# Kernel tuning notes

Hardware: AMD Instinct MI355X
Metric: run time of the kernel (lower is better)

## Reference

```python
import jax, jax.numpy as jnp
import numpy as np

NEG_SLOPE_GAT = 0.2   # GATConv internal leaky_relu slope (PyG default)
NEG_SLOPE = 0.01      # nn.LeakyReLU default slope


def _gat(h_src_in, h_dst_in, src, dst, Wsrc, Wdst, a_s, a_d, b, n_dst, self_loops):
    """Single-head PyG-style GATConv: gather -> score -> edge softmax -> scatter-sum."""
    hs = h_src_in @ Wsrc            # [N_src, C]
    hd = h_dst_in @ Wdst            # [N_dst, C]
    if self_loops:                  # static flag; same node set on both sides
        loop = jnp.arange(n_dst, dtype=src.dtype)
        src = jnp.concatenate([src, loop])
        dst = jnp.concatenate([dst, loop])
    # attention logits per edge
    e = jax.nn.leaky_relu((hs @ a_s)[src] + (hd @ a_d)[dst], NEG_SLOPE_GAT)  # [E]
    # softmax over edges sharing a destination node
    m = jax.ops.segment_max(e, dst, num_segments=n_dst)
    ex = jnp.exp(e - m[dst])
    denom = jax.ops.segment_sum(ex, dst, num_segments=n_dst)
    alpha = ex / denom[dst]
    out = jax.ops.segment_sum(hs[src] * alpha[:, None], dst, num_segments=n_dst)
    return out + b


def setup_inputs() -> dict:
    key = jax.random.key(0)
    ks = iter(jax.random.split(key, 64))
    NB, NP = 100_000, 50_000
    E_bb, E_pp, E_bp = 800_000, 400_000, 400_000
    FB, FP, H, H2 = 32, 34, 64, 32
    rn = lambda shape, s=0.05: jax.random.normal(next(ks), shape, jnp.float32) * s
    d = {}
    d['x_b'] = rn((NB, FB), 1.0)
    d['x_p'] = rn((NP, FP), 1.0)
    d['ei_bb'] = jax.random.randint(next(ks), (2, E_bb), 0, NB, jnp.int32)
    d['ei_pp'] = jax.random.randint(next(ks), (2, E_pp), 0, NP, jnp.int32)
    d['ei_bp_src'] = jax.random.randint(next(ks), (E_bp,), 0, NB, jnp.int32)
    d['ei_bp_dst'] = jax.random.randint(next(ks), (E_bp,), 0, NP, jnp.int32)
    d['W_in_b'] = rn((FB, H)); d['b_in_b'] = jnp.zeros((H,), jnp.float32)
    d['W_in_p'] = rn((FP, H)); d['b_in_p'] = jnp.zeros((H,), jnp.float32)
    for tag, cin, cout in (('1', H, H), ('2', H, H2)):
        d['W_bb' + tag] = rn((cin, cout)); d['as_bb' + tag] = rn((cout,)); d['ad_bb' + tag] = rn((cout,)); d['b_bb' + tag] = jnp.zeros((cout,), jnp.float32)
        d['W_pp' + tag] = rn((cin, cout)); d['as_pp' + tag] = rn((cout,)); d['ad_pp' + tag] = rn((cout,)); d['b_pp' + tag] = jnp.zeros((cout,), jnp.float32)
        d['Ws_bp' + tag] = rn((cin, cout)); d['Wd_bp' + tag] = rn((cin, cout)); d['as_bp' + tag] = rn((cout,)); d['ad_bp' + tag] = rn((cout,)); d['b_bp' + tag] = jnp.zeros((cout,), jnp.float32)
    d['W_out'] = rn((H2, 1)); d['b_out'] = jnp.zeros((1,), jnp.float32)
    return d


def reference(x_b, x_p, ei_bb, ei_pp, ei_bp_src, ei_bp_dst,
              W_in_b, b_in_b, W_in_p, b_in_p,
              W_bb1, as_bb1, ad_bb1, b_bb1, W_pp1, as_pp1, ad_pp1, b_pp1,
              Ws_bp1, Wd_bp1, as_bp1, ad_bp1, b_bp1,
              W_bb2, as_bb2, ad_bb2, b_bb2, W_pp2, as_pp2, ad_pp2, b_pp2,
              Ws_bp2, Wd_bp2, as_bp2, ad_bp2, b_bp2,
              W_out, b_out):
    NB, NP = x_b.shape[0], x_p.shape[0]
    lr = lambda v: jax.nn.leaky_relu(v, NEG_SLOPE)
    # input projections (dropout is eval-mode identity)
    hb = lr(x_b @ W_in_b + b_in_b)
    hp = lr(x_p @ W_in_p + b_in_p)
    # hetero conv 1 (sum aggregation over relations sharing a dst type)
    ob = _gat(hb, hb, ei_bb[0], ei_bb[1], W_bb1, W_bb1, as_bb1, ad_bb1, b_bb1, NB, True)
    op = (_gat(hp, hp, ei_pp[0], ei_pp[1], W_pp1, W_pp1, as_pp1, ad_pp1, b_pp1, NP, True)
          + _gat(hb, hp, ei_bp_src, ei_bp_dst, Ws_bp1, Wd_bp1, as_bp1, ad_bp1, b_bp1, NP, False))
    hb, hp = lr(ob), lr(op)
    # hetero conv 2
    ob2 = _gat(hb, hb, ei_bb[0], ei_bb[1], W_bb2, W_bb2, as_bb2, ad_bb2, b_bb2, NB, True)
    op2 = (_gat(hp, hp, ei_pp[0], ei_pp[1], W_pp2, W_pp2, as_pp2, ad_pp2, b_pp2, NP, True)
           + _gat(hb, hp, ei_bp_src, ei_bp_dst, Ws_bp2, Wd_bp2, as_bp2, ad_bp2, b_bp2, NP, False))
    hp = lr(op2)
    return hp @ W_out + b_out  # [NP, 1]
```

## Files before the change

kernel.cpp:

```cpp
#include <hip/hip_runtime.h>
#include <hip/hip_bf16.h>
#include <cstdint>
#include <cstddef>


typedef __attribute__((ext_vector_type(8))) short short8;
typedef __attribute__((ext_vector_type(4))) float f32x4;
typedef unsigned int u32;
typedef __hip_bfloat16 bf16;

#define ABITS 9
#define CHUNKE 8192

static __device__ __forceinline__ float ldf(const void* p, int i, int bf) {
    return bf ? __bfloat162float(((const bf16*)p)[i]) : ((const float*)p)[i];
}

static __device__ __forceinline__ short f2bs(float f) {
    bf16 h = __float2bfloat16(f);
    return *reinterpret_cast<short*>(&h);
}
static __device__ __forceinline__ float bs2f(short s) {
    bf16 h = *reinterpret_cast<bf16*>(&s);
    return __bfloat162float(h);
}
static __device__ __forceinline__ float lo16(u32 u) { return bs2f((short)(u & 0xffffu)); }
static __device__ __forceinline__ float hi16(u32 u) { return bs2f((short)(u >> 16)); }
static __device__ __forceinline__ u32 pack2(float x, float y) {
    return (u32)(unsigned short)f2bs(x) | ((u32)(unsigned short)f2bs(y) << 16);
}
static __device__ __forceinline__ float sel4(const float* a, int i) {
    return i == 0 ? a[0] : i == 1 ? a[1] : i == 2 ? a[2] : a[3];
}
static __device__ __forceinline__ float lrelu2(float x) { return x > 0.f ? x : 0.2f * x; }

static __device__ __forceinline__ int probe_bf(const unsigned* __restrict__ w, int* cnt) {
    if (threadIdx.x == 0) *cnt = 0;
    __syncthreads();
    int c = 0;
#pragma unroll
    for (int j = 0; j < 4; ++j) {
        unsigned u = w[threadIdx.x * 4 + j];
        unsigned e = (u >> 7) & 0xffu;
        c += (e >= 100u && e <= 145u) ? 1 : 0;
    }
    atomicAdd(cnt, c);
    __syncthreads();
    int r = (*cnt > 614) ? 1 : 0;
    __syncthreads();
    return r;
}

__global__ __launch_bounds__(256) void k_fv(
    const unsigned* __restrict__ probe_w, int* __restrict__ flag,
    const void* W_bb1, const void* as_bb1, const void* ad_bb1,
    const void* Ws_bp1, const void* as_bp1,
    const void* W_pp1, const void* as_pp1, const void* ad_pp1,
    const void* Wd_bp1, const void* ad_bp1,
    float* __restrict__ FVg)
{
    __shared__ int cnt;
    int bf = probe_bf(probe_w, &cnt);
    if (threadIdx.x == 0) *flag = bf;
    int lane = threadIdx.x & 63, wv = threadIdx.x >> 6;
    const void* Ws[6] = { W_bb1, W_bb1, Ws_bp1, W_pp1, W_pp1, Wd_bp1 };
    const void* av[6] = { as_bb1, ad_bb1, as_bp1, as_pp1, ad_pp1, ad_bp1 };
#pragma unroll
    for (int v = 0; v < 6; ++v) {
        float a = ldf(av[v], lane, bf);
        for (int k = wv; k < 64; k += 4) {
            float p = ldf(Ws[v], k * 64 + lane, bf) * a;
#pragma unroll
            for (int off = 1; off < 64; off <<= 1) p += __shfl_xor(p, off);
            if (lane == 0) FVg[v * 64 + k] = p;
        }
    }
}

template <int CIN>
static __device__ __forceinline__ void in_proj_body(
    short* WT, float* bl, float* FV, int bid,
    const void* __restrict__ X, const void* __restrict__ W, const void* __restrict__ B,
    const float* __restrict__ FVg,
    bf16* __restrict__ Y,
    float* __restrict__ S0, float* __restrict__ S1v, float* __restrict__ S2v,
    int M, int bf)
{
    constexpr int KP = 40;
    for (int i = threadIdx.x; i < 64 * CIN; i += 256) {
        int n = i / CIN, k = i - n * CIN;
        WT[n * KP + k] = f2bs(ldf(W, k * 64 + n, bf));
    }
    if (threadIdx.x < 64) bl[threadIdx.x] = ldf(B, threadIdx.x, bf);
    if (threadIdx.x < 192) FV[threadIdx.x] = FVg[threadIdx.x];
    __syncthreads();

    int lane = threadIdx.x & 63;
    int wv   = threadIdx.x >> 6;
    int m = lane & 15, quad = lane >> 4;
    int row0 = (bid * 4 + wv) * 16;
    if (row0 >= M) return;

    int arow = row0 + m; if (arow >= M) arow = M - 1;
    short8 a;
#pragma unroll
    for (int j = 0; j < 8; ++j)
        a[j] = f2bs(ldf(X, arow * CIN + quad * 8 + j, bf));

    f32x4 acc[4] = {};
#pragma unroll
    for (int tt = 0; tt < 4; ++tt) {
        short8 bfr = *(const short8*)&WT[((lane & 15) + 16 * tt) * KP + quad * 8];
        acc[tt] = __builtin_amdgcn_mfma_f32_16x16x32_bf16(a, bfr, acc[tt], 0, 0, 0);
    }

    if (CIN == 34) {
        float x32[4], x33[4];
#pragma unroll
        for (int r = 0; r < 4; ++r) {
            int row = row0 + quad * 4 + r; if (row >= M) row = M - 1;
            x32[r] = ldf(X, row * CIN + 32, bf);
            x33[r] = ldf(X, row * CIN + 33, bf);
        }
#pragma unroll
        for (int tt = 0; tt < 4; ++tt) {
            int col = (lane & 15) + 16 * tt;
            float w32 = bs2f(WT[col * KP + 32]);
            float w33 = bs2f(WT[col * KP + 33]);
#pragma unroll
            for (int r = 0; r < 4; ++r)
                acc[tt][r] += x32[r] * w32 + x33[r] * w33;
        }
    }

    float vs[4] = {}, vd[4] = {}, ve[4] = {};
#pragma unroll
    for (int tt = 0; tt < 4; ++tt) {
        int col = (lane & 15) + 16 * tt;
        float bb = bl[col];
        float w0 = FV[col], w1 = FV[64 + col], w2 = FV[128 + col];
#pragma unroll
        for (int r = 0; r < 4; ++r) {
            int row = row0 + quad * 4 + r;
            float v = acc[tt][r] + bb;
            v = v > 0.f ? v : 0.01f * v;
            if (row < M) Y[(size_t)row * 64 + col] = __float2bfloat16(v);
            vs[r] += v * w0; vd[r] += v * w1; ve[r] += v * w2;
        }
    }
#pragma unroll
    for (int off = 1; off < 16; off <<= 1)
#pragma unroll
        for (int r = 0; r < 4; ++r) {
            vs[r] += __shfl_xor(vs[r], off);
            vd[r] += __shfl_xor(vd[r], off);
            ve[r] += __shfl_xor(ve[r], off);
        }
    int c = lane & 15;
    int row = row0 + quad * 4 + (c & 3);
    if (row < M && c < 12) {
        if (c < 4)       S0[row]  = sel4(vs, c & 3);
        else if (c < 8)  S1v[row] = sel4(vd, c & 3);
        else             S2v[row] = sel4(ve, c & 3);
    }
}

__global__ __launch_bounds__(256) void k_hist_projp(
    const int* __restrict__ bb_d, const int* __restrict__ pp_d,
    const int* __restrict__ bp_d, int* __restrict__ histM,
    int E_bb, int E_pp, int E_bp, int NB, int NP, int nbkt, int nblk,
    const void* __restrict__ Xp, const void* __restrict__ Wp, const void* __restrict__ Bp,
    bf16* __restrict__ Yp, int MP,
    const float* __restrict__ FVg, const int* __restrict__ flag,
    float* __restrict__ ss_pp, float* __restrict__ sd_pp, float* __restrict__ sd_bp)
{
    __shared__ short WT[64 * 40];
    __shared__ float bl[64];
    __shared__ float FV[192];
    __shared__ int aux[1 << ABITS];
    if ((int)blockIdx.x < nblk) {
        for (int i = threadIdx.x; i < nbkt; i += 256) aux[i] = 0;
        __syncthreads();
        int E_all = E_bb + E_pp + E_bp;
        int base = blockIdx.x * CHUNKE;
        int end = base + CHUNKE < E_all ? base + CHUNKE : E_all;
        for (int i = base + threadIdx.x; i < end; i += 256) {
            int d;
            if (i < E_bb) d = bb_d[i];
            else if (i < E_bb + E_pp) d = NB + pp_d[i - E_bb];
            else d = NB + NP + bp_d[i - E_bb - E_pp];
            atomicAdd(&aux[d >> ABITS], 1);
        }
        __syncthreads();
        for (int i = threadIdx.x; i < nbkt; i += 256)
            histM[(size_t)i * nblk + blockIdx.x] = aux[i];
    } else {
        const int bfv = *flag;
        int bid = blockIdx.x - nblk;
        in_proj_body<34>(WT, bl, FV, bid, Xp, Wp, Bp, FVg + 192,
            Yp, ss_pp, sd_pp, sd_bp, MP, bfv);
    }
}

__global__ __launch_bounds__(1024) void k_scan1(const int* __restrict__ deg,
                                                int* __restrict__ out,
                                                int* __restrict__ bsum, int n)
{
    __shared__ int wsum[16];
    int gid = blockIdx.x * 1024 + threadIdx.x;
    int lane = threadIdx.x & 63, wid = threadIdx.x >> 6;
    int v = (gid < n) ? deg[gid] : 0;
    int x = v;
#pragma unroll
    for (int off = 1; off < 64; off <<= 1) {
        int y = __shfl_up(x, off, 64);
        if (lane >= off) x += y;
    }
    if (lane == 63) wsum[wid] = x;
    __syncthreads();
    if (wid == 0 && lane < 16) {
        int w0 = wsum[lane];
#pragma unroll
        for (int off = 1; off < 16; off <<= 1) {
            int y = __shfl_up(w0, off, 16);
            if (lane >= off) w0 += y;
        }
        wsum[lane] = w0;
    }
    __syncthreads();
    int base = (wid > 0) ? wsum[wid - 1] : 0;
    int incl = base + x;
    if (gid < n) out[gid] = incl - v;
    if (threadIdx.x == 1023) bsum[blockIdx.x] = incl;
}

__global__ __launch_bounds__(1024) void k_scan2(int* __restrict__ bsum, int nb)
{
    __shared__ int wsum[16];
    int lane = threadIdx.x & 63, wid = threadIdx.x >> 6;
    int v = (threadIdx.x < nb) ? bsum[threadIdx.x] : 0;
    int x = v;
#pragma unroll
    for (int off = 1; off < 64; off <<= 1) {
        int y = __shfl_up(x, off, 64);
        if (lane >= off) x += y;
    }
    if (lane == 63) wsum[wid] = x;
    __syncthreads();
    if (wid == 0 && lane < 16) {
        int w0 = wsum[lane];
#pragma unroll
        for (int off = 1; off < 16; off <<= 1) {
            int y = __shfl_up(w0, off, 16);
            if (lane >= off) w0 += y;
        }
        wsum[lane] = w0;
    }
    __syncthreads();
    int base = (wid > 0) ? wsum[wid - 1] : 0;
    if (threadIdx.x < nb) bsum[threadIdx.x] = base + x - v;
}

__global__ __launch_bounds__(1024) void k_scan3(int* __restrict__ indptr,
                                                const int* __restrict__ bsum,
                                                int n, int E)
{
    int gid = blockIdx.x * 1024 + threadIdx.x;
    if (gid < n) indptr[gid] += bsum[blockIdx.x];
    if (gid == 0) indptr[n] = E;
}

__global__ __launch_bounds__(256) void k_scatter_projb(
    const int* __restrict__ bb_s, const int* __restrict__ bb_d,
    const int* __restrict__ pp_s, const int* __restrict__ pp_d,
    const int* __restrict__ bp_s, const int* __restrict__ bp_d,
    const int* __restrict__ histS, unsigned* __restrict__ ebuf,
    int E_bb, int E_pp, int E_bp, int NB, int NP, int nbkt, int nblk,
    const void* __restrict__ Xb, const void* __restrict__ Wb, const void* __restrict__ Bb,
    bf16* __restrict__ Yb, int MB,
    const float* __restrict__ FVg, const int* __restrict__ flag,
    float* __restrict__ ss_bb, float* __restrict__ sd_bb, float* __restrict__ ss_bp)
{
    __shared__ short WT[64 * 40];
    __shared__ float bl[64];
    __shared__ float FV[192];
    if ((int)blockIdx.x < nblk) {
        int* cur = (int*)WT;
        for (int i = threadIdx.x; i < nbkt; i += 256)
            cur[i] = histS[(size_t)i * nblk + blockIdx.x];
        __syncthreads();
        int E_all = E_bb + E_pp + E_bp;
        int base = blockIdx.x * CHUNKE;
        int end = base + CHUNKE < E_all ? base + CHUNKE : E_all;
        for (int i = base + threadIdx.x; i < end; i += 256) {
            int s, d;
            if (i < E_bb) { s = bb_s[i]; d = bb_d[i]; }
            else if (i < E_bb + E_pp) { int j = i - E_bb; s = pp_s[j]; d = NB + pp_d[j]; }
            else { int j = i - E_bb - E_pp; s = bp_s[j]; d = NB + NP + bp_d[j]; }
            int p = atomicAdd(&cur[d >> ABITS], 1);
            ebuf[p] = ((unsigned)(d & ((1 << ABITS) - 1)) << 20) | (unsigned)s;
        }
    } else {
        const int bfv = *flag;
        int bid = blockIdx.x - nblk;
        in_proj_body<32>(WT, bl, FV, bid, Xb, Wb, Bb, FVg,
            Yb, ss_bb, sd_bb, ss_bp, MB, bfv);
    }
}

__global__ __launch_bounds__(256) void k_finalize(
    const unsigned* __restrict__ ebuf, const int* __restrict__ histS,
    int* __restrict__ ip_all, unsigned* __restrict__ sw2,
    int NALL, int E_all, int nbkt, int nblk)
{
    __shared__ int h[1 << ABITS];
    __shared__ int pre[1 << ABITS];
    __shared__ int wq[4];
    int b = blockIdx.x;
    int d0 = b << ABITS;
    int nloc = NALL - d0 < (1 << ABITS) ? NALL - d0 : (1 << ABITS);
    int t = threadIdx.x;
    for (int i = t; i < (1 << ABITS); i += 256) h[i] = 0;
    __syncthreads();
    int s0 = histS[(size_t)b * nblk];
    int s1 = histS[(size_t)(b + 1) * nblk];
    for (int i = s0 + t; i < s1; i += 256)
        atomicAdd(&h[ebuf[i] >> 20], 1);
    __syncthreads();
    int v0 = h[2 * t], v1 = h[2 * t + 1];
    int ps = v0 + v1;
    int lane = t & 63, wid = t >> 6;
    int x = ps;
#pragma unroll
    for (int off = 1; off < 64; off <<= 1) {
        int y = __shfl_up(x, off, 64);
        if (lane >= off) x += y;
    }
    if (lane == 63) wq[wid] = x;
    __syncthreads();
    if (t == 0) {
        int a = 0;
#pragma unroll
        for (int w = 0; w < 4; ++w) { int tmp = wq[w]; wq[w] = a; a += tmp; }
    }
    __syncthreads();
    int excl = wq[wid] + x - ps;
    pre[2 * t]     = excl;
    pre[2 * t + 1] = excl + v0;
    __syncthreads();
    for (int i = t; i < nloc; i += 256) ip_all[d0 + i] = s0 + pre[i];
    if (d0 + nloc == NALL && t == 0) ip_all[NALL] = E_all;
    for (int i = t; i < (1 << ABITS); i += 256) h[i] = s0 + pre[i];
    __syncthreads();
    for (int i = s0 + t; i < s1; i += 256) {
        unsigned e = ebuf[i];
        int dl = (int)(e >> 20);
        int p = atomicAdd(&h[dl], 1);
        sw2[p] = e & 0xFFFFFu;
    }
}

static __device__ __forceinline__ void gather1_body(
    int bid, const int* __restrict__ ip, const unsigned* __restrict__ sw2,
    const float* __restrict__ SS, const float* __restrict__ SD,
    const bf16* __restrict__ HS, bf16* __restrict__ OUT, int M)
{
    int lane = threadIdx.x & 63;
    int half = lane >> 5, hl = lane & 31;
    int d = bid * 4 + (threadIdx.x >> 6);
    if (d >= M) return;
    const u32* H32 = (const u32*)HS;
    float sdd = SD[d];
    float ax = 0.f, ay = 0.f, den = 0.f;
    if (half == 0) {
        float ex = __expf(lrelu2(SS[d] + sdd));
        u32 h = H32[(size_t)d * 32 + hl];
        ax = lo16(h) * ex; ay = hi16(h) * ex; den = ex;
    }
    int j1 = ip[d + 1];
    int j = ip[d] + half;
    for (; j + 6 < j1; j += 8) {
        int s0 = (int)sw2[j], s1 = (int)sw2[j + 2];
        int s2 = (int)sw2[j + 4], s3 = (int)sw2[j + 6];
        u32 h0 = H32[(size_t)s0 * 32 + hl];
        u32 h1 = H32[(size_t)s1 * 32 + hl];
        u32 h2 = H32[(size_t)s2 * 32 + hl];
        u32 h3 = H32[(size_t)s3 * 32 + hl];
        float e0 = __expf(lrelu2(SS[s0] + sdd));
        float e1 = __expf(lrelu2(SS[s1] + sdd));
        float e2 = __expf(lrelu2(SS[s2] + sdd));
        float e3 = __expf(lrelu2(SS[s3] + sdd));
        ax += lo16(h0) * e0 + lo16(h1) * e1 + lo16(h2) * e2 + lo16(h3) * e3;
        ay += hi16(h0) * e0 + hi16(h1) * e1 + hi16(h2) * e2 + hi16(h3) * e3;
        den += (e0 + e1) + (e2 + e3);
    }
    for (; j < j1; j += 2) {
        int s0 = (int)sw2[j];
        u32 h0 = H32[(size_t)s0 * 32 + hl];
        float e0 = __expf(lrelu2(SS[s0] + sdd));
        ax += lo16(h0) * e0; ay += hi16(h0) * e0; den += e0;
    }
    ax += __shfl_xor(ax, 32); ay += __shfl_xor(ay, 32); den += __shfl_xor(den, 32);
    if (half == 0) {
        float inv = 1.f / den;
        ((u32*)OUT)[(size_t)d * 32 + hl] = pack2(ax * inv, ay * inv);
    }
}

static __device__ __forceinline__ void gather2_body(
    int bid, const int* __restrict__ ip1, const unsigned* __restrict__ sw2,
    const float* __restrict__ SS1, const float* __restrict__ SD1,
    const bf16* __restrict__ H1T,
    const int* __restrict__ ip2,
    const float* __restrict__ SSb, const float* __restrict__ SDb,
    const bf16* __restrict__ H2T,
    bf16* __restrict__ O1, bf16* __restrict__ O2, int M)
{
    int lane = threadIdx.x & 63;
    int half = lane >> 5, hl = lane & 31;
    int d = bid * 4 + (threadIdx.x >> 6);
    if (d >= M) return;
    const u32* H1 = (const u32*)H1T;
    const u32* H2 = (const u32*)H2T;
    float sdd1 = SD1[d];
    float a1x = 0.f, a1y = 0.f, den1 = 0.f;
    if (half == 0) {
        float ex = __expf(lrelu2(SS1[d] + sdd1));
        u32 h = H1[(size_t)d * 32 + hl];
        a1x = lo16(h) * ex; a1y = hi16(h) * ex; den1 = ex;
    }
    int j1 = ip1[d + 1];
    int j = ip1[d] + half;
    for (; j + 6 < j1; j += 8) {
        int s0 = (int)sw2[j], s1 = (int)sw2[j + 2];
        int s2 = (int)sw2[j + 4], s3 = (int)sw2[j + 6];
        u32 h0 = H1[(size_t)s0 * 32 + hl];
        u32 h1 = H1[(size_t)s1 * 32 + hl];
        u32 h2 = H1[(size_t)s2 * 32 + hl];
        u32 h3 = H1[(size_t)s3 * 32 + hl];
        float e0 = __expf(lrelu2(SS1[s0] + sdd1));
        float e1 = __expf(lrelu2(SS1[s1] + sdd1));
        float e2 = __expf(lrelu2(SS1[s2] + sdd1));
        float e3 = __expf(lrelu2(SS1[s3] + sdd1));
        a1x += lo16(h0) * e0 + lo16(h1) * e1 + lo16(h2) * e2 + lo16(h3) * e3;
        a1y += hi16(h0) * e0 + hi16(h1) * e1 + hi16(h2) * e2 + hi16(h3) * e3;
        den1 += (e0 + e1) + (e2 + e3);
    }
    for (; j < j1; j += 2) {
        int s0 = (int)sw2[j];
        u32 h0 = H1[(size_t)s0 * 32 + hl];
        float e0 = __expf(lrelu2(SS1[s0] + sdd1));
        a1x += lo16(h0) * e0; a1y += hi16(h0) * e0; den1 += e0;
    }
    float sdd2 = SDb[d];
    float a2x = 0.f, a2y = 0.f, den2 = 0.f;
    j1 = ip2[d + 1];
    j = ip2[d] + half;
    for (; j + 6 < j1; j += 8) {
        int s0 = (int)sw2[j], s1 = (int)sw2[j + 2];
        int s2 = (int)sw2[j + 4], s3 = (int)sw2[j + 6];
        u32 h0 = H2[(size_t)s0 * 32 + hl];
        u32 h1 = H2[(size_t)s1 * 32 + hl];
        u32 h2 = H2[(size_t)s2 * 32 + hl];
        u32 h3 = H2[(size_t)s3 * 32 + hl];
        float e0 = __expf(lrelu2(SSb[s0] + sdd2));
        float e1 = __expf(lrelu2(SSb[s1] + sdd2));
        float e2 = __expf(lrelu2(SSb[s2] + sdd2));
        float e3 = __expf(lrelu2(SSb[s3] + sdd2));
        a2x += lo16(h0) * e0 + lo16(h1) * e1 + lo16(h2) * e2 + lo16(h3) * e3;
        a2y += hi16(h0) * e0 + hi16(h1) * e1 + hi16(h2) * e2 + hi16(h3) * e3;
        den2 += (e0 + e1) + (e2 + e3);
    }
    for (; j < j1; j += 2) {
        int s0 = (int)sw2[j];
        u32 h0 = H2[(size_t)s0 * 32 + hl];
        float e0 = __expf(lrelu2(SSb[s0] + sdd2));
        a2x += lo16(h0) * e0; a2y += hi16(h0) * e0; den2 += e0;
    }
    a1x += __shfl_xor(a1x, 32); a1y += __shfl_xor(a1y, 32); den1 += __shfl_xor(den1, 32);
    a2x += __shfl_xor(a2x, 32); a2y += __shfl_xor(a2y, 32); den2 += __shfl_xor(den2, 32);
    if (half == 0) {
        float inv1 = 1.f / den1;
        float inv2 = den2 > 0.f ? 1.f / den2 : 0.f;
        ((u32*)O1)[(size_t)d * 32 + hl] = pack2(a1x * inv1, a1y * inv1);
        ((u32*)O2)[(size_t)d * 32 + hl] = pack2(a2x * inv2, a2y * inv2);
    }
}

__global__ __launch_bounds__(256) void k_gather12(
    const int* __restrict__ ip_bb, const unsigned* __restrict__ sw2,
    const float* __restrict__ ss_bb, const float* __restrict__ sd_bb,
    const bf16* __restrict__ hb, bf16* __restrict__ agg_bb, int NB,
    const int* __restrict__ ip_pp, const int* __restrict__ ip_bp,
    const float* __restrict__ ss_pp, const float* __restrict__ sd_pp,
    const float* __restrict__ ss_bp, const float* __restrict__ sd_bp,
    const bf16* __restrict__ hp,
    bf16* __restrict__ agg_pp, bf16* __restrict__ agg_bp, int NP)
{
    int nbb = (NB + 3) >> 2;
    if ((int)blockIdx.x < nbb)
        gather1_body(blockIdx.x, ip_bb, sw2, ss_bb, sd_bb, hb, agg_bb, NB);
    else
        gather2_body(blockIdx.x - nbb, ip_pp, sw2, ss_pp, sd_pp, hp,
                     ip_bp, ss_bp, sd_bp, hb, agg_pp, agg_bp, NP);
}

template <bool D1, bool D2>
static __device__ __forceinline__ void fused_body(
    short* WT1, short* WT2, short* HT, float* bl, int bid,
    const bf16* __restrict__ A1, const bf16* __restrict__ A2,
    const void* W1a, const void* W1b, const void* B1a, const void* B1b,
    const void* W2a, const void* W2b,
    const void* av0, const void* av1, const void* av2,
    bf16* __restrict__ HS,
    float* __restrict__ S0, float* __restrict__ S1v, float* __restrict__ S2v,
    int M, int bf)
{
    constexpr int KP = 72;
    for (int i = threadIdx.x; i < 64 * 64; i += 256) {
        int n = i >> 6, k = i & 63;
        WT1[n * KP + k] = f2bs(ldf(W1a, k * 64 + n, bf));
        if (D1) WT1[(64 + n) * KP + k] = f2bs(ldf(W1b, k * 64 + n, bf));
    }
    for (int i = threadIdx.x; i < 32 * 64; i += 256) {
        int n = i >> 6, k = i & 63;
        WT2[n * KP + k] = f2bs(ldf(W2a, k * 32 + n, bf));
        if (D2) WT2[(32 + n) * KP + k] = f2bs(ldf(W2b, k * 32 + n, bf));
    }
    if (threadIdx.x < 64) {
        float b = ldf(B1a, threadIdx.x, bf);
        if (D1) b += ldf(B1b, threadIdx.x, bf);
        bl[threadIdx.x] = b;
    }
    __syncthreads();

    int lane = threadIdx.x & 63;
    int wv   = threadIdx.x >> 6;
    int m = lane & 15, quad = lane >> 4;
    int row0 = (bid * 4 + wv) * 16;
    bool act = row0 < M;

    const short* A1s = (const short*)A1;
    const short* A2s = (const short*)A2;
    if (act) {
        int arow = row0 + m; if (arow >= M) arow = M - 1;
        f32x4 acc[4] = {};
#pragma unroll
        for (int ks = 0; ks < 2; ++ks) {
            short8 a1 = *(const short8*)&A1s[(size_t)arow * 64 + ks * 32 + quad * 8];
#pragma unroll
            for (int tt = 0; tt < 4; ++tt) {
                short8 bfr = *(const short8*)&WT1[((lane & 15) + 16 * tt) * KP + ks * 32 + quad * 8];
                acc[tt] = __builtin_amdgcn_mfma_f32_16x16x32_bf16(a1, bfr, acc[tt], 0, 0, 0);
            }
            if (D1) {
                short8 a2 = *(const short8*)&A2s[(size_t)arow * 64 + ks * 32 + quad * 8];
#pragma unroll
                for (int tt = 0; tt < 4; ++tt) {
                    short8 bfr = *(const short8*)&WT1[(64 + (lane & 15) + 16 * tt) * KP + ks * 32 + quad * 8];
                    acc[tt] = __builtin_amdgcn_mfma_f32_16x16x32_bf16(a2, bfr, acc[tt], 0, 0, 0);
                }
            }
        }
#pragma unroll
        for (int tt = 0; tt < 4; ++tt) {
            int col = (lane & 15) + 16 * tt;
            float bb = bl[col];
#pragma unroll
            for (int r = 0; r < 4; ++r) {
                float v = acc[tt][r] + bb;
                v = v > 0.f ? v : 0.01f * v;
                HT[(wv * 16 + quad * 4 + r) * 80 + col] = f2bs(v);
            }
        }
    }
    __syncthreads();

    f32x4 acc2[D2 ? 4 : 2] = {};
    if (act) {
        int arow = row0 + m; if (arow >= M) arow = M - 1;
        int al = arow - bid * 64;
#pragma unroll
        for (int ks = 0; ks < 2; ++ks) {
            short8 a = *(const short8*)&HT[al * 80 + ks * 32 + quad * 8];
#pragma unroll
            for (int tt = 0; tt < (D2 ? 4 : 2); ++tt) {
                short8 bfr = *(const short8*)&WT2[((lane & 15) + 16 * tt) * KP + ks * 32 + quad * 8];
                acc2[tt] = __builtin_amdgcn_mfma_f32_16x16x32_bf16(a, bfr, acc2[tt], 0, 0, 0);
            }
        }
    }

    float vs[4] = {}, vd[4] = {}, ve[4] = {};
#pragma unroll
    for (int tt = 0; tt < 2; ++tt) {
        int col = (lane & 15) + 16 * tt;
        float a0 = ldf(av0, col, bf);
#pragma unroll
        for (int r = 0; r < 4; ++r) vs[r] += acc2[tt][r] * a0;
        if (D1) {
            float a1 = ldf(av1, col, bf);
#pragma unroll
            for (int r = 0; r < 4; ++r) vd[r] += acc2[tt][r] * a1;
        }
    }
    if (D2) {
#pragma unroll
        for (int tt = 0; tt < 2; ++tt) {
            int col = (lane & 15) + 16 * tt;
            float a2 = ldf(av2, col, bf);
#pragma unroll
            for (int r = 0; r < 4; ++r) ve[r] += acc2[2 + tt][r] * a2;
        }
    }
#pragma unroll
    for (int off = 1; off < 16; off <<= 1)
#pragma unroll
        for (int r = 0; r < 4; ++r) {
            vs[r] += __shfl_xor(vs[r], off);
            if (D1) vd[r] += __shfl_xor(vd[r], off);
            if (D2) ve[r] += __shfl_xor(ve[r], off);
        }
    int c = lane & 15;
    int row = row0 + quad * 4 + (c & 3);
    if (act && row < M) {
        if (c < 4)                    S0[row]  = sel4(vs, c & 3);
        else if (D1 && c < 8)         S1v[row] = sel4(vd, c & 3);
        else if (D2 && c >= 8 && c < 12) S2v[row] = sel4(ve, c & 3);
    }
    if (act) {
#pragma unroll
        for (int tt = 0; tt < 2; ++tt) {
            int col = (lane & 15) + 16 * tt;
#pragma unroll
            for (int r = 0; r < 4; ++r) {
                int row2 = row0 + quad * 4 + r;
                if (row2 < M)
                    HS[(size_t)row2 * 32 + col] = __float2bfloat16(acc2[tt][r]);
            }
        }
    }
}

__global__ __launch_bounds__(256) void k_fused_proj(
    const bf16* __restrict__ agg_pp, const bf16* __restrict__ agg_bp,
    const void* W_pp1, const void* Ws_bp1, const void* b_pp1, const void* b_bp1,
    const void* W_pp2, const void* Wd_bp2,
    const void* as_pp2, const void* ad_pp2, const void* ad_bp2,
    bf16* __restrict__ hs2_pp, float* __restrict__ ss2_pp,
    float* __restrict__ sd2_pp, float* __restrict__ sd2_bp, int MP,
    const bf16* __restrict__ agg_bb, const void* W_bb1, const void* b_bb1,
    const void* Ws_bp2, const void* as_bp2,
    bf16* __restrict__ hs2_bp, float* __restrict__ ss2_bp, int MB,
    const int* __restrict__ flag)
{
    const int bf = *flag;
    __shared__ __align__(16) short WT1[128 * 72];
    __shared__ __align__(16) short WT2[64 * 72];
    __shared__ __align__(16) short HT[64 * 80];
    __shared__ float bl[64];
    int npb = (MP + 63) >> 6;
    if ((int)blockIdx.x < npb)
        fused_body<true, true>(WT1, WT2, HT, bl, blockIdx.x,
            agg_pp, agg_bp, W_pp1, Ws_bp1, b_pp1, b_bp1,
            W_pp2, Wd_bp2, as_pp2, ad_pp2, ad_bp2,
            hs2_pp, ss2_pp, sd2_pp, sd2_bp, MP, bf);
    else
        fused_body<false, false>(WT1, WT2, HT, bl, blockIdx.x - npb,
            agg_bb, nullptr, W_bb1, nullptr, b_bb1, nullptr,
            Ws_bp2, nullptr, as_bp2, nullptr, nullptr,
            hs2_bp, ss2_bp, nullptr, nullptr, MB, bf);
}

__global__ __launch_bounds__(256) void k_gather_out(
    const int* __restrict__ ip1, const unsigned* __restrict__ sw2,
    const float* __restrict__ SS1, const float* __restrict__ SD1,
    const bf16* __restrict__ HS1,
    const int* __restrict__ ip2,
    const float* __restrict__ SS2, const float* __restrict__ SD2,
    const bf16* __restrict__ HS2,
    const void* __restrict__ b1, const void* __restrict__ b2,
    const void* __restrict__ Wout, const void* __restrict__ bout,
    void* __restrict__ OUT, int M, const int* __restrict__ flag)
{
    const int bf = *flag;
    int lane = threadIdx.x & 63;
    int q = lane >> 4, hl = lane & 15;
    int d = blockIdx.x * 4 + (threadIdx.x >> 6);
    if (d >= M) return;
    const u32* H1 = (const u32*)HS1;
    const u32* H2 = (const u32*)HS2;
    float sdd = SD1[d];
    float a1x = 0.f, a1y = 0.f, den1 = 0.f;
    if (q == 0) {
        float ex = __expf(lrelu2(SS1[d] + sdd));
        u32 h = H1[(size_t)d * 16 + hl];
        a1x = lo16(h) * ex; a1y = hi16(h) * ex; den1 = ex;
    }
    int j1 = ip1[d + 1];
    int j = ip1[d] + q;
    for (; j + 4 < j1; j += 8) {
        int s0 = (int)sw2[j], s1 = (int)sw2[j + 4];
        u32 h0 = H1[(size_t)s0 * 16 + hl];
        u32 h1 = H1[(size_t)s1 * 16 + hl];
        float e0 = __expf(lrelu2(SS1[s0] + sdd));
        float e1 = __expf(lrelu2(SS1[s1] + sdd));
        a1x += lo16(h0) * e0 + lo16(h1) * e1;
        a1y += hi16(h0) * e0 + hi16(h1) * e1;
        den1 += e0 + e1;
    }
    if (j < j1) {
        int s0 = (int)sw2[j];
        u32 h0 = H1[(size_t)s0 * 16 + hl];
        float e0 = __expf(lrelu2(SS1[s0] + sdd));
        a1x += lo16(h0) * e0; a1y += hi16(h0) * e0; den1 += e0;
    }
    float sdd2 = SD2[d];
    float a2x = 0.f, a2y = 0.f, den2 = 0.f;
    j1 = ip2[d + 1];
    j = ip2[d] + q;
    for (; j + 4 < j1; j += 8) {
        int s0 = (int)sw2[j], s1 = (int)sw2[j + 4];
        u32 h0 = H2[(size_t)s0 * 16 + hl];
        u32 h1 = H2[(size_t)s1 * 16 + hl];
        float e0 = __expf(lrelu2(SS2[s0] + sdd2));
        float e1 = __expf(lrelu2(SS2[s1] + sdd2));
        a2x += lo16(h0) * e0 + lo16(h1) * e1;
        a2y += hi16(h0) * e0 + hi16(h1) * e1;
        den2 += e0 + e1;
    }
    if (j < j1) {
        int s0 = (int)sw2[j];
        u32 h0 = H2[(size_t)s0 * 16 + hl];
        float e0 = __expf(lrelu2(SS2[s0] + sdd2));
        a2x += lo16(h0) * e0; a2y += hi16(h0) * e0; den2 += e0;
    }
    a1x += __shfl_xor(a1x, 16); a1y += __shfl_xor(a1y, 16); den1 += __shfl_xor(den1, 16);
    a2x += __shfl_xor(a2x, 16); a2y += __shfl_xor(a2y, 16); den2 += __shfl_xor(den2, 16);
    a1x += __shfl_xor(a1x, 32); a1y += __shfl_xor(a1y, 32); den1 += __shfl_xor(den1, 32);
    a2x += __shfl_xor(a2x, 32); a2y += __shfl_xor(a2y, 32); den2 += __shfl_xor(den2, 32);
    float inv2 = den2 > 0.f ? 1.f / den2 : 0.f;
    float vx = a1x / den1 + a2x * inv2 + ldf(b1, 2 * hl, bf) + ldf(b2, 2 * hl, bf);
    float vy = a1y / den1 + a2y * inv2 + ldf(b1, 2 * hl + 1, bf) + ldf(b2, 2 * hl + 1, bf);
    vx = vx > 0.f ? vx : 0.01f * vx;
    vy = vy > 0.f ? vy : 0.01f * vy;
    float t = vx * ldf(Wout, 2 * hl, bf) + vy * ldf(Wout, 2 * hl + 1, bf);
#pragma unroll
    for (int off = 1; off < 16; off <<= 1) t += __shfl_xor(t, off);
    if (lane == 0) {
        float r = t + ldf(bout, 0, bf);
        if (bf) ((bf16*)OUT)[d] = __float2bfloat16(r);
        else    ((float*)OUT)[d] = r;
    }
}

extern "C" void kernel_launch(void* const* d_in, const int* in_sizes, int n_in,
                              void* d_out, int out_size, void* d_ws, size_t ws_size,
                              hipStream_t stream)
{
    const void* x_b = d_in[0];
    const void* x_p = d_in[1];
    const int* ei_bb = (const int*)d_in[2];
    const int* ei_pp = (const int*)d_in[3];
    const int* bp_s  = (const int*)d_in[4];
    const int* bp_d  = (const int*)d_in[5];
    const void *W_in_b = d_in[6],  *b_in_b = d_in[7];
    const void *W_in_p = d_in[8],  *b_in_p = d_in[9];
    const void *W_bb1 = d_in[10], *as_bb1 = d_in[11], *ad_bb1 = d_in[12], *b_bb1 = d_in[13];
    const void *W_pp1 = d_in[14], *as_pp1 = d_in[15], *ad_pp1 = d_in[16], *b_pp1 = d_in[17];
    const void *Ws_bp1 = d_in[18], *Wd_bp1 = d_in[19], *as_bp1 = d_in[20], *ad_bp1 = d_in[21], *b_bp1 = d_in[22];
    const void *W_pp2 = d_in[27], *as_pp2 = d_in[28], *ad_pp2 = d_in[29], *b_pp2 = d_in[30];
    const void *Ws_bp2 = d_in[31], *Wd_bp2 = d_in[32], *as_bp2 = d_in[33], *ad_bp2 = d_in[34], *b_bp2 = d_in[35];
    const void *W_out = d_in[36], *b_out = d_in[37];

    const int NB   = in_sizes[0] / 32;
    const int NP   = in_sizes[1] / 34;
    const int E_bb = in_sizes[2] / 2;
    const int E_pp = in_sizes[3] / 2;
    const int E_bp = in_sizes[4];
    const int E_all = E_bb + E_pp + E_bp;
    const int NALL  = NB + 2 * NP;
    const int* bb_s = ei_bb;  const int* bb_d = ei_bb + E_bb;
    const int* pp_s = ei_pp;  const int* pp_d = ei_pp + E_pp;
    (void)ws_size; (void)n_in; (void)out_size;

    const int nbkt  = (NALL + (1 << ABITS) - 1) >> ABITS;
    const int nblk  = (E_all + CHUNKE - 1) / CHUNKE;
    const int nh    = nbkt * nblk;

    char* base = (char*)d_ws;
    size_t o = 0;
    auto alloc = [&](size_t bytes) { char* p = base + o; o += (bytes + 255) & ~(size_t)255; return p; };

    int* flag  = (int*)alloc(256);
    float* FVg = (float*)alloc(6 * 64 * 4);
    int* bsum  = (int*)alloc(1024 * 4);
    int* histM = (int*)alloc((size_t)nh * 4);
    int* histS = (int*)alloc((size_t)(nh + 1) * 4);
    int* ip_all = (int*)alloc((size_t)(NALL + 1) * 4);
    unsigned* ebuf = (unsigned*)alloc((size_t)E_all * 4);
    unsigned* sw2  = (unsigned*)alloc((size_t)E_all * 4);
    float* ss_bb = (float*)alloc((size_t)NB * 4);
    float* sd_bb = (float*)alloc((size_t)NB * 4);
    float* ss_bp = (float*)alloc((size_t)NB * 4);
    float* ss_pp = (float*)alloc((size_t)NP * 4);
    float* sd_pp = (float*)alloc((size_t)NP * 4);
    float* sd_bp = (float*)alloc((size_t)NP * 4);
    float* ss2_bp = ss_bb;
    float* ss2_pp = ss_pp;
    float* sd2_pp = sd_pp;
    float* sd2_bp = sd_bp;

    char* S1 = alloc((size_t)NB * 64 * 2);
    char* S2 = alloc((size_t)NP * 64 * 2);
    char* S3 = alloc((size_t)NB * 64 * 2);
    char* S5 = alloc((size_t)NP * 64 * 2);
    char* S6 = alloc((size_t)NP * 64 * 2);

    bf16* hb     = (bf16*)S1;
    bf16* hp     = (bf16*)S2;
    bf16* agg_bb = (bf16*)S3;
    bf16* agg_bp = (bf16*)S5;
    bf16* agg_pp = (bf16*)S6;
    bf16* hs2_pp = (bf16*)S2;
    bf16* hs2_bp = (bf16*)S1;

    auto cdiv = [](int a, int b) { return (a + b - 1) / b; };

    const int* ip_bb = ip_all;
    const int* ip_pp = ip_all + NB;
    const int* ip_bp = ip_all + NB + NP;

    k_fv<<<1, 256, 0, stream>>>(
        (const unsigned*)x_b, flag,
        W_bb1, as_bb1, ad_bb1, Ws_bp1, as_bp1,
        W_pp1, as_pp1, ad_pp1, Wd_bp1, ad_bp1, FVg);

    k_hist_projp<<<nblk + cdiv(NP, 64), 256, 0, stream>>>(
        bb_d, pp_d, bp_d, histM,
        E_bb, E_pp, E_bp, NB, NP, nbkt, nblk,
        x_p, W_in_p, b_in_p, hp, NP,
        FVg, flag, ss_pp, sd_pp, sd_bp);

    int sb1 = cdiv(nh, 1024);
    k_scan1<<<sb1, 1024, 0, stream>>>(histM, histS, bsum, nh);
    k_scan2<<<1, 1024, 0, stream>>>(bsum, sb1);
    k_scan3<<<sb1, 1024, 0, stream>>>(histS, bsum, nh, E_all);

    k_scatter_projb<<<nblk + cdiv(NB, 64), 256, 0, stream>>>(
        bb_s, bb_d, pp_s, pp_d, bp_s, bp_d, histS, ebuf,
        E_bb, E_pp, E_bp, NB, NP, nbkt, nblk,
        x_b, W_in_b, b_in_b, hb, NB,
        FVg, flag, ss_bb, sd_bb, ss_bp);

    k_finalize<<<nbkt, 256, 0, stream>>>(ebuf, histS, ip_all, sw2,
                                         NALL, E_all, nbkt, nblk);

    k_gather12<<<cdiv(NB, 4) + cdiv(NP, 4), 256, 0, stream>>>(
        ip_bb, sw2, ss_bb, sd_bb, hb, agg_bb, NB,
        ip_pp, ip_bp, ss_pp, sd_pp, ss_bp, sd_bp, hp, agg_pp, agg_bp, NP);

    k_fused_proj<<<cdiv(NP, 64) + cdiv(NB, 64), 256, 0, stream>>>(
        agg_pp, agg_bp, W_pp1, Ws_bp1, b_pp1, b_bp1,
        W_pp2, Wd_bp2, as_pp2, ad_pp2, ad_bp2,
        hs2_pp, ss2_pp, sd2_pp, sd2_bp, NP,
        agg_bb, W_bb1, b_bb1, Ws_bp2, as_bp2,
        hs2_bp, ss2_bp, NB, flag);

    k_gather_out<<<cdiv(NP, 4), 256, 0, stream>>>(
        ip_pp, sw2, ss2_pp, sd2_pp, hs2_pp,
        ip_bp, ss2_bp, sd2_bp, hs2_bp,
        b_pp2, b_bp2, W_out, b_out, d_out, NP, flag);
}
```

Before: 406.6 us.

## Fuse histogram into weight-folding kernel and single-block scan into projection kernel

```diff
diff --git a/kernel.cpp b/kernel.cpp
--- a/kernel.cpp
+++ b/kernel.cpp
@@ -10,7 +10,7 @@
 typedef __hip_bfloat16 bf16;
 
 #define ABITS 9
-#define CHUNKE 8192
+#define CHUNKE 16384
 
 static __device__ __forceinline__ float ldf(const void* p, int i, int bf) {
     return bf ? __bfloat162float(((const bf16*)p)[i]) : ((const float*)p)[i];
@@ -51,30 +51,52 @@
     return r;
 }
 
-__global__ __launch_bounds__(256) void k_fv(
+__global__ __launch_bounds__(256) void k_fv_hist(
     const unsigned* __restrict__ probe_w, int* __restrict__ flag,
     const void* W_bb1, const void* as_bb1, const void* ad_bb1,
     const void* Ws_bp1, const void* as_bp1,
     const void* W_pp1, const void* as_pp1, const void* ad_pp1,
     const void* Wd_bp1, const void* ad_bp1,
-    float* __restrict__ FVg)
-{
-    __shared__ int cnt;
-    int bf = probe_bf(probe_w, &cnt);
-    if (threadIdx.x == 0) *flag = bf;
-    int lane = threadIdx.x & 63, wv = threadIdx.x >> 6;
-    const void* Ws[6] = { W_bb1, W_bb1, Ws_bp1, W_pp1, W_pp1, Wd_bp1 };
-    const void* av[6] = { as_bb1, ad_bb1, as_bp1, as_pp1, ad_pp1, ad_bp1 };
-#pragma unroll
-    for (int v = 0; v < 6; ++v) {
-        float a = ldf(av[v], lane, bf);
-        for (int k = wv; k < 64; k += 4) {
-            float p = ldf(Ws[v], k * 64 + lane, bf) * a;
-#pragma unroll
-            for (int off = 1; off < 64; off <<= 1) p += __shfl_xor(p, off);
-            if (lane == 0) FVg[v * 64 + k] = p;
-        }
-    }
+    float* __restrict__ FVg,
+    const int* __restrict__ bb_d, const int* __restrict__ pp_d,
+    const int* __restrict__ bp_d, int* __restrict__ histM,
+    int E_bb, int E_pp, int E_bp, int NB, int NP, int nbkt, int nblk)
+{
+    __shared__ int aux[1 << ABITS];
+    if (blockIdx.x == 0) {
+        int bf = probe_bf(probe_w, &aux[0]);
+        if (threadIdx.x == 0) *flag = bf;
+        int lane = threadIdx.x & 63, wv = threadIdx.x >> 6;
+        const void* Ws[6] = { W_bb1, W_bb1, Ws_bp1, W_pp1, W_pp1, Wd_bp1 };
+        const void* av[6] = { as_bb1, ad_bb1, as_bp1, as_pp1, ad_pp1, ad_bp1 };
+#pragma unroll
+        for (int v = 0; v < 6; ++v) {
+            float a = ldf(av[v], lane, bf);
+            for (int k = wv; k < 64; k += 4) {
+                float p = ldf(Ws[v], k * 64 + lane, bf) * a;
+#pragma unroll
+                for (int off = 1; off < 64; off <<= 1) p += __shfl_xor(p, off);
+                if (lane == 0) FVg[v * 64 + k] = p;
+            }
+        }
+        return;
+    }
+    int blk = blockIdx.x - 1;
+    for (int i = threadIdx.x; i < nbkt; i += 256) aux[i] = 0;
+    __syncthreads();
+    int E_all = E_bb + E_pp + E_bp;
+    int base = blk * CHUNKE;
+    int end = base + CHUNKE < E_all ? base + CHUNKE : E_all;
+    for (int i = base + threadIdx.x; i < end; i += 256) {
+        int d;
+        if (i < E_bb) d = bb_d[i];
+        else if (i < E_bb + E_pp) d = NB + pp_d[i - E_bb];
+        else d = NB + NP + bp_d[i - E_bb - E_pp];
+        atomicAdd(&aux[d >> ABITS], 1);
+    }
+    __syncthreads();
+    for (int i = threadIdx.x; i < nbkt; i += 256)
+        histM[(size_t)i * nblk + blk] = aux[i];
 }
 
 template <int CIN>
@@ -165,10 +187,8 @@
     }
 }
 
-__global__ __launch_bounds__(256) void k_hist_projp(
-    const int* __restrict__ bb_d, const int* __restrict__ pp_d,
-    const int* __restrict__ bp_d, int* __restrict__ histM,
-    int E_bb, int E_pp, int E_bp, int NB, int NP, int nbkt, int nblk,
+__global__ __launch_bounds__(256) void k_scan_projp(
+    const int* __restrict__ histM, int* __restrict__ histS, int nh, int E_all,
     const void* __restrict__ Xp, const void* __restrict__ Wp, const void* __restrict__ Bp,
     bf16* __restrict__ Yp, int MP,
     const float* __restrict__ FVg, const int* __restrict__ flag,
@@ -177,97 +197,42 @@
     __shared__ short WT[64 * 40];
     __shared__ float bl[64];
     __shared__ float FV[192];
-    __shared__ int aux[1 << ABITS];
-    if ((int)blockIdx.x < nblk) {
-        for (int i = threadIdx.x; i < nbkt; i += 256) aux[i] = 0;
+    __shared__ int wsum[4];
+    __shared__ int carry;
+    if (blockIdx.x == 0) {
+        if (threadIdx.x == 0) carry = 0;
         __syncthreads();
-        int E_all = E_bb + E_pp + E_bp;
-        int base = blockIdx.x * CHUNKE;
-        int end = base + CHUNKE < E_all ? base + CHUNKE : E_all;
-        for (int i = base + threadIdx.x; i < end; i += 256) {
-            int d;
-            if (i < E_bb) d = bb_d[i];
-            else if (i < E_bb + E_pp) d = NB + pp_d[i - E_bb];
-            else d = NB + NP + bp_d[i - E_bb - E_pp];
-            atomicAdd(&aux[d >> ABITS], 1);
-        }
-        __syncthreads();
-        for (int i = threadIdx.x; i < nbkt; i += 256)
-            histM[(size_t)i * nblk + blockIdx.x] = aux[i];
-    } else {
-        const int bfv = *flag;
-        int bid = blockIdx.x - nblk;
-        in_proj_body<34>(WT, bl, FV, bid, Xp, Wp, Bp, FVg + 192,
-            Yp, ss_pp, sd_pp, sd_bp, MP, bfv);
-    }
-}
-
-__global__ __launch_bounds__(1024) void k_scan1(const int* __restrict__ deg,
-                                                int* __restrict__ out,
-                                                int* __restrict__ bsum, int n)
-{
-    __shared__ int wsum[16];
-    int gid = blockIdx.x * 1024 + threadIdx.x;
-    int lane = threadIdx.x & 63, wid = threadIdx.x >> 6;
-    int v = (gid < n) ? deg[gid] : 0;
-    int x = v;
-#pragma unroll
-    for (int off = 1; off < 64; off <<= 1) {
-        int y = __shfl_up(x, off, 64);
-        if (lane >= off) x += y;
-    }
-    if (lane == 63) wsum[wid] = x;
-    __syncthreads();
-    if (wid == 0 && lane < 16) {
-        int w0 = wsum[lane];
-#pragma unroll
-        for (int off = 1; off < 16; off <<= 1) {
-            int y = __shfl_up(w0, off, 16);
-            if (lane >= off) w0 += y;
-        }
-        wsum[lane] = w0;
-    }
-    __syncthreads();
-    int base = (wid > 0) ? wsum[wid - 1] : 0;
-    int incl = base + x;
-    if (gid < n) out[gid] = incl - v;
-    if (threadIdx.x == 1023) bsum[blockIdx.x] = incl;
-}
-
-__global__ __launch_bounds__(1024) void k_scan2(int* __restrict__ bsum, int nb)
-{
-    __shared__ int wsum[16];
-    int lane = threadIdx.x & 63, wid = threadIdx.x >> 6;
-    int v = (threadIdx.x < nb) ? bsum[threadIdx.x] : 0;
-    int x = v;
-#pragma unroll
-    for (int off = 1; off < 64; off <<= 1) {
-        int y = __shfl_up(x, off, 64);
-        if (lane >= off) x += y;
-    }
-    if (lane == 63) wsum[wid] = x;
-    __syncthreads();
-    if (wid == 0 && lane < 16) {
-        int w0 = wsum[lane];
-#pragma unroll
-        for (int off = 1; off < 16; off <<= 1) {
-            int y = __shfl_up(w0, off, 16);
-            if (lane >= off) w0 += y;
-        }
-        wsum[lane] = w0;
-    }
-    __syncthreads();
-    int base = (wid > 0) ? wsum[wid - 1] : 0;
-    if (threadIdx.x < nb) bsum[threadIdx.x] = base + x - v;
-}
-
-__global__ __launch_bounds__(1024) void k_scan3(int* __restrict__ indptr,
-                                                const int* __restrict__ bsum,
-                                                int n, int E)
-{
-    int gid = blockIdx.x * 1024 + threadIdx.x;
-    if (gid < n) indptr[gid] += bsum[blockIdx.x];
-    if (gid == 0) indptr[n] = E;
+        for (int base = 0; base < nh; base += 256) {
+            int gid = base + threadIdx.x;
+            int v = (gid < nh) ? histM[gid] : 0;
+            int lane = threadIdx.x & 63, wid = threadIdx.x >> 6;
+            int x = v;
+#pragma unroll
+            for (int off = 1; off < 64; off <<= 1) {
+                int y = __shfl_up(x, off, 64);
+                if (lane >= off) x += y;
+            }
+            if (lane == 63) wsum[wid] = x;
+            __syncthreads();
+            if (threadIdx.x == 0) {
+                int a = 0;
+#pragma unroll
+                for (int w = 0; w < 4; ++w) { int tmp = wsum[w]; wsum[w] = a; a += tmp; }
+            }
+            __syncthreads();
+            int excl = carry + wsum[wid] + x - v;
+            if (gid < nh) histS[gid] = excl;
+            __syncthreads();
+            if (threadIdx.x == 255) carry = excl + v;
+            __syncthreads();
+        }
+        if (threadIdx.x == 0) histS[nh] = E_all;
+        return;
+    }
+    const int bfv = *flag;
+    int bid = blockIdx.x - 1;
+    in_proj_body<34>(WT, bl, FV, bid, Xp, Wp, Bp, FVg + 192,
+        Yp, ss_pp, sd_pp, sd_bp, MP, bfv);
 }
 
 __global__ __launch_bounds__(256) void k_scatter_projb(
@@ -794,7 +759,6 @@
 
     int* flag  = (int*)alloc(256);
     float* FVg = (float*)alloc(6 * 64 * 4);
-    int* bsum  = (int*)alloc(1024 * 4);
     int* histM = (int*)alloc((size_t)nh * 4);
     int* histS = (int*)alloc((size_t)(nh + 1) * 4);
     int* ip_all = (int*)alloc((size_t)(NALL + 1) * 4);
@@ -831,21 +795,16 @@
     const int* ip_pp = ip_all + NB;
     const int* ip_bp = ip_all + NB + NP;
 
-    k_fv<<<1, 256, 0, stream>>>(
+    k_fv_hist<<<1 + nblk, 256, 0, stream>>>(
         (const unsigned*)x_b, flag,
         W_bb1, as_bb1, ad_bb1, Ws_bp1, as_bp1,
-        W_pp1, as_pp1, ad_pp1, Wd_bp1, ad_bp1, FVg);
-
-    k_hist_projp<<<nblk + cdiv(NP, 64), 256, 0, stream>>>(
-        bb_d, pp_d, bp_d, histM,
-        E_bb, E_pp, E_bp, NB, NP, nbkt, nblk,
+        W_pp1, as_pp1, ad_pp1, Wd_bp1, ad_bp1, FVg,
+        bb_d, pp_d, bp_d, histM, E_bb, E_pp, E_bp, NB, NP, nbkt, nblk);
+
+    k_scan_projp<<<1 + cdiv(NP, 64), 256, 0, stream>>>(
+        histM, histS, nh, E_all,
         x_p, W_in_p, b_in_p, hp, NP,
         FVg, flag, ss_pp, sd_pp, sd_bp);
-
-    int sb1 = cdiv(nh, 1024);
-    k_scan1<<<sb1, 1024, 0, stream>>>(histM, histS, bsum, nh);
-    k_scan2<<<1, 1024, 0, stream>>>(bsum, sb1);
-    k_scan3<<<sb1, 1024, 0, stream>>>(histS, bsum, nh, E_all);
 
     k_scatter_projb<<<nblk + cdiv(NB, 64), 256, 0, stream>>>(
         bb_s, bb_d, pp_s, pp_d, bp_s, bp_d, histS, ebuf,
```

Result: slower. 503.5 us (+23.8%).
